# Kernel optimization log

Hardware: AMD Instinct MI355X
Metric: run time of the kernel (lower is better)

## Reference

```python
import jax, jax.numpy as jnp
import numpy as np
from jax import lax

DIST_THRESH = 180.0
ATT_THRESH = 0.05


def setup_inputs() -> dict:
    key = jax.random.key(0)
    ks = jax.random.split(key, 6)
    B, N, H, W = 16, 512, 25, 25
    F, Fh = H * W, int(H * W * 1.5)  # 625, 937
    x4 = jax.random.normal(ks[0], (B, N, H, W), dtype=jnp.float32) * 0.25
    attention = jax.random.uniform(ks[1], (B, N, 1, 1), dtype=jnp.float32)
    W1 = jax.random.normal(ks[2], (2, F, Fh), dtype=jnp.float32) * (1.0 / np.sqrt(F))
    b1 = jnp.zeros((Fh,), dtype=jnp.float32)
    W2 = jax.random.normal(ks[3], (2, Fh, F), dtype=jnp.float32) * (1.0 / np.sqrt(Fh))
    b2 = jnp.zeros((F,), dtype=jnp.float32)
    return {"x4": x4, "attention": attention, "W1": W1, "b1": b1, "W2": W2, "b2": b2}


def _build_adjacency(X, att):
    """X: [B,N,F] node features, att: [B,N]. Returns thresholded adjacency [B,N,N]."""
    B, N, F = X.shape
    # pairwise L1 distances, row-by-row scan to avoid materializing [B,N,N,F]
    Xs = jnp.swapaxes(X, 0, 1)  # [N,B,F]

    def row(_, xi):  # xi: [B,F]
        d = jnp.sum(jnp.abs(xi[:, None, :] - X), axis=-1)  # [B,N]
        return None, d

    _, D = lax.scan(row, None, Xs)          # [N,B,N]
    D = jnp.swapaxes(D, 0, 1)               # [B,N,N]
    att_d = jnp.abs(att[:, :, None] - att[:, None, :])  # [B,N,N]
    A = ((D <= DIST_THRESH) & (att_d <= ATT_THRESH)).astype(jnp.float32)
    # original only fills i<j and j<i, diagonal stays 0
    A = A * (1.0 - jnp.eye(N, dtype=jnp.float32))
    return A


def _process_graph(A):
    """A + I, then row-normalize by inverse degree (D^-1 (A+I))."""
    N = A.shape[1]
    A = A + jnp.eye(N, dtype=A.dtype)
    deg = jnp.sum(A, axis=-1)               # [B,N]
    dinv = jnp.where(deg > 0, 1.0 / deg, 0.0)
    return dinv[:, :, None] * A


def _cheb_conv(x, L, Wk, b):
    """ChebConv with K=2 over dense normalized graph L: T0=x, T1=Lx."""
    t1 = jnp.einsum('bij,bjf->bif', L, x)
    return jnp.einsum('bnf,fo->bno', x, Wk[0]) + jnp.einsum('bnf,fo->bno', t1, Wk[1]) + b


def reference(x4, attention, W1, b1, W2, b2):
    B, N, H, W = x4.shape
    X = x4.reshape(B, N, H * W)             # [B,N,625] flow_x
    att = attention[:, :, 0, 0]             # [B,N]
    A = _build_adjacency(X, att)
    L = _process_graph(A)
    h = jax.nn.relu(_cheb_conv(X, L, W1, b1))   # [B,N,937]
    out = jax.nn.relu(_cheb_conv(h, L, W2, b2))  # [B,N,625]
    return out
```

## Files before the change

### kernel.cpp

```cpp
#include <hip/hip_runtime.h>
#include <stdint.h>

typedef uint16_t u16;
typedef uint32_t u32;
typedef __attribute__((ext_vector_type(4))) float f32x4;
typedef __attribute__((ext_vector_type(4))) unsigned short us4;
typedef __attribute__((ext_vector_type(8))) unsigned short us8;

#define NB   16
#define NN   512
#define FF   625
#define FH   937
#define ROWS 8192
#define KS1  1280
#define KS2  1920
#define NPX  640
#define NPH  960
#define F4   160
#define ITILE 8

using frag_ab = __attribute__((ext_vector_type(8))) short;
using frag_cd = __attribute__((ext_vector_type(4))) float;

__device__ __forceinline__ u16 f32_bf16(float f) {
  union { float f; uint32_t u; } x; x.f = f;
  uint32_t r = x.u + 0x7fffu + ((x.u >> 16) & 1u);
  return (u16)(r >> 16);
}
__device__ __forceinline__ void gload_lds16(const void* g, void* l) {
  __builtin_amdgcn_global_load_lds((__attribute__((address_space(1))) void*)g,
                                   (__attribute__((address_space(3))) void*)l,
                                   16, 0, 0);
}

__global__ __launch_bounds__(256) void prep(
    const float* __restrict__ x4, const float* __restrict__ att,
    const float* __restrict__ W1, const float* __restrict__ W2,
    f32x4* __restrict__ Xpad, u16* __restrict__ Xcat, u16* __restrict__ Xt,
    u16* __restrict__ W1t, u16* __restrict__ W2t,
    float* __restrict__ att_s, u16* __restrict__ ord_g)
{
  const int blk = blockIdx.x;
  const int tid = threadIdx.x;
  if (blk < 4096) {
    const int xcd = blk & 7, loc = blk >> 3;
    const int row0 = xcd * 1024 + loc * 2;
    for (int s = tid; s < 320; s += 256) {
      const int row = row0 + (s >= 160);
      const int k4 = (s >= 160) ? s - 160 : s;
      f32x4 v; us4 o;
      #pragma unroll
      for (int t = 0; t < 4; ++t) {
        const int f = k4 * 4 + t;
        float x = (f < FF) ? x4[(size_t)row * FF + f] : 0.f;
        v[t] = x; o[t] = f32_bf16(x);
      }
      Xpad[(size_t)row * F4 + k4] = v;
      *(us4*)(Xcat + (size_t)row * KS1 + k4 * 4) = o;
    }
  } else if (blk < 9216) {
    __shared__ float tile[32][33];
    const int bb = blk - 4096;
    const int xcd = bb & 7, sub = bb >> 3;
    const int b = xcd * 2 + sub / 320;
    const int t = sub % 320;
    const int ft = t % 20, kt = t / 20;
    const int tx = tid & 31, ty = tid >> 5;
    #pragma unroll
    for (int r = 0; r < 4; ++r) {
      const int node = kt * 32 + ty + r * 8;
      const int f = ft * 32 + tx;
      tile[ty + r * 8][tx] = (f < FF) ? x4[((size_t)b * NN + node) * FF + f] : 0.f;
    }
    __syncthreads();
    #pragma unroll
    for (int r = 0; r < 4; ++r) {
      const int f = ft * 32 + ty + r * 8;
      const int node = kt * 32 + tx;
      Xt[((size_t)b * NPX + f) * 512 + node] = f32_bf16(tile[tx][ty + r * 8]);
    }
  } else if (blk < 10496) {
    __shared__ float tile[32][33];
    const int bb = blk - 9216;
    const int kt = bb % 40, nt = bb / 40;
    const int tx = tid & 31, ty = tid >> 5;
    #pragma unroll
    for (int r = 0; r < 4; ++r) {
      int k = kt * 32 + ty + r * 8;
      int n = nt * 32 + tx;
      float v = 0.f;
      int c = -1, kk = 0;
      if (k < 625) { c = 0; kk = k; }
      else if (k >= 640 && k < 1265) { c = 1; kk = k - 640; }
      if (c >= 0 && n < FH) v = W1[((size_t)c * 625 + kk) * FH + n];
      tile[ty + r * 8][tx] = v;
    }
    __syncthreads();
    #pragma unroll
    for (int r = 0; r < 4; ++r) {
      int n = nt * 32 + ty + r * 8;
      int k = kt * 32 + tx;
      W1t[(size_t)n * KS1 + k] = f32_bf16(tile[tx][ty + r * 8]);
    }
  } else if (blk < 11696) {
    __shared__ float tile[32][33];
    const int bb = blk - 10496;
    const int kt = bb % 60, nt = bb / 60;
    const int tx = tid & 31, ty = tid >> 5;
    #pragma unroll
    for (int r = 0; r < 4; ++r) {
      int k = kt * 32 + ty + r * 8;
      int n = nt * 32 + tx;
      float v = 0.f;
      int c = -1, kk = 0;
      if (k < 937) { c = 0; kk = k; }
      else if (k >= 960 && k < 1897) { c = 1; kk = k - 960; }
      if (c >= 0 && n < FF) v = W2[((size_t)c * 937 + kk) * FF + n];
      tile[ty + r * 8][tx] = v;
    }
    __syncthreads();
    #pragma unroll
    for (int r = 0; r < 4; ++r) {
      int n = nt * 32 + ty + r * 8;
      int k = kt * 32 + tx;
      W2t[(size_t)n * KS2 + k] = f32_bf16(tile[tx][ty + r * 8]);
    }
  } else {
    __shared__ float sa[512];
    __shared__ u16 so[512];
    const int b = blk - 11696;
    sa[tid] = att[b * NN + tid]; sa[tid + 256] = att[b * NN + tid + 256];
    so[tid] = (u16)tid; so[tid + 256] = (u16)(tid + 256);
    for (int k = 2; k <= 512; k <<= 1) {
      for (int j = k >> 1; j > 0; j >>= 1) {
        __syncthreads();
        const int i = ((tid & ~(j - 1)) << 1) | (tid & (j - 1));
        const int p = i | j;
        const bool up = ((i & k) == 0);
        const float va = sa[i], vp = sa[p];
        if ((va > vp) == up) {
          sa[i] = vp; sa[p] = va;
          const u16 t = so[i]; so[i] = so[p]; so[p] = t;
        }
      }
    }
    __syncthreads();
    att_s[b * NN + tid] = sa[tid]; att_s[b * NN + tid + 256] = sa[tid + 256];
    ord_g[b * NN + tid] = so[tid]; ord_g[b * NN + tid + 256] = so[tid + 256];
  }
}

__global__ __launch_bounds__(256) void build_L_tiled(
    const f32x4* __restrict__ Xpad,
    const float* __restrict__ att_s, const u16* __restrict__ ord_g,
    u16* __restrict__ L)
{
  __shared__ f32x4 Xi[ITILE][F4];
  __shared__ float as_[512];
  __shared__ u16 ord[512];
  __shared__ u32 mask[ITILE][16];
  __shared__ int deg[ITILE];
  __shared__ int jlo_s, jhi_s;
  __shared__ u16 dvs[ITILE];

  const int tid = threadIdx.x;
  const int blk = blockIdx.x;
  const int xcd = blk & 7, sub = blk >> 3;
  const int b = xcd * 2 + (sub >> 6);
  const int it = sub & 63;
  const int s0 = it * ITILE;
  const f32x4* Xb4 = Xpad + (size_t)b * NN * F4;

  as_[tid] = att_s[b * NN + tid]; as_[tid + 256] = att_s[b * NN + tid + 256];
  ord[tid] = ord_g[b * NN + tid]; ord[tid + 256] = ord_g[b * NN + tid + 256];
  if (tid < ITILE * 16) ((u32*)mask)[tid] = 0;
  if (tid < ITILE) deg[tid] = 0;
  __syncthreads();

  for (int s = tid; s < ITILE * F4; s += 256) {
    const int ii = s / F4, k4 = s - ii * F4;
    Xi[ii][k4] = Xb4[(size_t)ord[s0 + ii] * F4 + k4];
  }
  if (tid == 0) {
    const float lot = as_[s0] - 0.05f;
    int lo = 0, hi = 512;
    while (lo < hi) { int m = (lo + hi) >> 1; if (as_[m] < lot) lo = m + 1; else hi = m; }
    jlo_s = lo;
  } else if (tid == 1) {
    const float hit = as_[s0 + ITILE - 1] + 0.05f;
    int lo = 0, hi = 512;
    while (lo < hi) { int m = (lo + hi) >> 1; if (as_[m] <= hit) lo = m + 1; else hi = m; }
    jhi_s = lo;
  }
  __syncthreads();

  const int hl = tid & 31;
  const int hw = tid >> 5;
  const int jlo = jlo_s, jhi = jhi_s;

  for (int sj = jlo + hw; sj < jhi; sj += 8) {
    const int oj = ord[sj];
    const f32x4* Xj = Xb4 + (size_t)oj * F4;
    const f32x4 xj0 = Xj[hl];
    const f32x4 xj1 = Xj[32 + hl];
    const f32x4 xj2 = Xj[64 + hl];
    const f32x4 xj3 = Xj[96 + hl];
    const f32x4 xj4 = Xj[128 + hl];
    const float aj = as_[sj];
    #pragma unroll 2
    for (int ii = 0; ii < ITILE; ++ii) {
      const int si = s0 + ii;
      if (si == sj || fabsf(aj - as_[si]) > 0.05f) continue;
      const f32x4 d0 = Xi[ii][hl] - xj0;
      const f32x4 d1 = Xi[ii][32 + hl] - xj1;
      const f32x4 d2 = Xi[ii][64 + hl] - xj2;
      const f32x4 d3 = Xi[ii][96 + hl] - xj3;
      const f32x4 d4 = Xi[ii][128 + hl] - xj4;
      float p = 0.f;
      #pragma unroll
      for (int t = 0; t < 4; ++t)
        p += fabsf(d0[t]) + fabsf(d1[t]) + fabsf(d2[t]) + fabsf(d3[t]) + fabsf(d4[t]);
      #pragma unroll
      for (int off = 16; off; off >>= 1) p += __shfl_xor(p, off, 64);
      if (hl == 0 && p <= 180.0f) {
        atomicOr(&mask[ii][sj >> 5], 1u << (sj & 31));
        atomicAdd(&deg[ii], 1);
      }
    }
  }
  __syncthreads();

  if (tid < ITILE) dvs[tid] = f32_bf16(1.0f / (float)(deg[tid] + 1));
  __syncthreads();

  if (tid < ITILE * 16) {
    const int ii = tid >> 4, w = tid & 15;
    const int oi = ord[s0 + ii];
    u16* Lrow = L + ((size_t)b * 512 + oi) * 512;
    const u16 dv = dvs[ii];
    u32 m = mask[ii][w];
    while (m) {
      const int bit = __ffs(m) - 1;
      m &= m - 1;
      Lrow[ord[w * 32 + bit]] = dv;
    }
    if (w == 0) Lrow[oi] = dv;
  }
}

template <int KS, int NTILE, int NREAL, int NSTORE, bool RELU, bool BIAS,
          bool OUT_BF16, bool TSTORE>
__device__ __forceinline__ void gemm_core(
    const u16* __restrict__ At, const u16* __restrict__ Btt,
    const float* __restrict__ bias, void* __restrict__ C,
    u16* __restrict__ tbuf, long crow0, int col0, int ldc)
{
  constexpr int NI = NTILE / 32;
  constexpr int BR = NTILE / 32;
  __shared__ __align__(16) u16 Ash[128 * 64];
  __shared__ __align__(16) u16 Bsh[NTILE * 64];

  const int tid  = threadIdx.x;
  const int lane = tid & 63;
  const int wave = tid >> 6;
  const int wm = wave & 1, wn = wave >> 1;
  const int q = lane >> 4, l16 = lane & 15;

  const u16* pa[4]; const u16* pb[BR];
  #pragma unroll
  for (int r = 0; r < 4; ++r) {
    const int ci = r * 256 + tid;
    const int row = ci >> 3, cpos = ci & 7;
    pa[r] = At + (size_t)row * KS + (cpos ^ (row & 7)) * 8;
  }
  #pragma unroll
  for (int r = 0; r < BR; ++r) {
    const int ci = r * 256 + tid;
    const int row = ci >> 3, cpos = ci & 7;
    pb[r] = Btt + (size_t)row * KS + (cpos ^ (row & 7)) * 8;
  }
  const int wbase = (tid & 192) * 8;

  const frag_ab* fA[4][2]; const frag_ab* fB[NI][2];
  #pragma unroll
  for (int mi = 0; mi < 4; ++mi) {
    const int row = wm * 64 + mi * 16 + l16;
    fA[mi][0] = (const frag_ab*)&Ash[row * 64 + ((q    ) ^ (l16 & 7)) * 8];
    fA[mi][1] = (const frag_ab*)&Ash[row * 64 + ((q + 4) ^ (l16 & 7)) * 8];
  }
  #pragma unroll
  for (int ni = 0; ni < NI; ++ni) {
    const int row = wn * (NTILE / 2) + ni * 16 + l16;
    fB[ni][0] = (const frag_ab*)&Bsh[row * 64 + ((q    ) ^ (l16 & 7)) * 8];
    fB[ni][1] = (const frag_ab*)&Bsh[row * 64 + ((q + 4) ^ (l16 & 7)) * 8];
  }

  frag_cd acc[4][NI] = {};

  constexpr int KT = KS / 64;
  for (int kt = 0; kt < KT; ++kt) {
    __syncthreads();
    #pragma unroll
    for (int r = 0; r < 4; ++r) { gload_lds16(pa[r], &Ash[r * 2048 + wbase]); pa[r] += 64; }
    #pragma unroll
    for (int r = 0; r < BR; ++r) { gload_lds16(pb[r], &Bsh[r * 2048 + wbase]); pb[r] += 64; }
    __syncthreads();

    #pragma unroll
    for (int kk = 0; kk < 2; ++kk) {
      frag_ab av[4], bv[NI];
      #pragma unroll
      for (int mi = 0; mi < 4; ++mi) av[mi] = *fA[mi][kk];
      #pragma unroll
      for (int ni = 0; ni < NI; ++ni) bv[ni] = *fB[ni][kk];
      #pragma unroll
      for (int mi = 0; mi < 4; ++mi)
        #pragma unroll
        for (int ni = 0; ni < NI; ++ni)
          acc[mi][ni] = __builtin_amdgcn_mfma_f32_16x16x32_bf16(
              av[mi], bv[ni], acc[mi][ni], 0, 0, 0);
    }
  }

  #pragma unroll
  for (int ni = 0; ni < NI; ++ni) {
    const int col = col0 + wn * (NTILE / 2) + ni * 16 + l16;
    if (col >= NSTORE) continue;
    const bool ok = (col < NREAL);
    float bvv = 0.f;
    if (BIAS) bvv = ok ? bias[col] : 0.f;
    #pragma unroll
    for (int mi = 0; mi < 4; ++mi) {
      #pragma unroll
      for (int r = 0; r < 4; ++r) {
        const long rowg = crow0 + wm * 64 + mi * 16 + q * 4 + r;
        float v = acc[mi][ni][r];
        if (BIAS) v += bvv;
        if (RELU) v = fmaxf(v, 0.f);
        if (!ok) v = 0.f;
        if (OUT_BF16) ((u16*)C)[rowg * (size_t)ldc + col] = f32_bf16(v);
        else          ((float*)C)[rowg * (size_t)ldc + col] = v;
        if (TSTORE) {
          tbuf[((size_t)(rowg >> 9) * NPH + col) * 512 + (rowg & 511)] = f32_bf16(v);
        }
      }
    }
  }
}

template <int KS, int NTILE, int NREAL, int NSTORE, bool RELU, bool BIAS,
          bool OUT_BF16, bool TSTORE>
__global__ __launch_bounds__(256) void gemm_dense(
    const u16* __restrict__ A, const u16* __restrict__ Bt,
    const float* __restrict__ bias, void* __restrict__ C,
    u16* __restrict__ tbuf, int ldc)
{
  const int x = blockIdx.x;
  const int mt = ((x & 7) << 3) | (x >> 3);
  gemm_core<KS, NTILE, NREAL, NSTORE, RELU, BIAS, OUT_BF16, TSTORE>(
      A + (size_t)mt * 128 * KS, Bt + (size_t)blockIdx.y * NTILE * KS,
      bias, C, tbuf, (long)mt * 128, blockIdx.y * NTILE, ldc);
}

template <int NP>
__global__ __launch_bounds__(256) void spmm(
    const u16* __restrict__ L, const u16* __restrict__ Bt,
    u16* __restrict__ C, int ldc)
{
  constexpr int TPB = 4 * (NP / 64);
  const int blk = blockIdx.x;
  const int xcd = blk & 7, sub = blk >> 3;
  const int b = xcd * 2 + sub / TPB;
  const int t = sub % TPB;
  const int mt = t & 3, nt = t >> 2;
  gemm_core<512, 64, NP, NP, false, false, true, false>(
      L + ((size_t)b * 512 + mt * 128) * 512,
      Bt + ((size_t)b * NP + nt * 64) * 512,
      nullptr, C, nullptr, (long)b * 512 + mt * 128, nt * 64, ldc);
}

extern "C" void kernel_launch(void* const* d_in, const int* in_sizes, int n_in,
                              void* d_out, int out_size, void* d_ws, size_t ws_size,
                              hipStream_t stream) {
  const float* x4  = (const float*)d_in[0];
  const float* att = (const float*)d_in[1];
  const float* W1  = (const float*)d_in[2];
  const float* b1  = (const float*)d_in[3];
  const float* W2  = (const float*)d_in[4];
  const float* b2  = (const float*)d_in[5];
  float* out = (float*)d_out;

  char* ws = (char*)d_ws;
  f32x4* Xpad = (f32x4*)ws;
  u16* ht = (u16*)ws;       ws += (size_t)ROWS * F4 * 16;
  u16* Xcat = (u16*)ws;  ws += (size_t)ROWS * KS1 * 2;
  u16* hcat = (u16*)ws;  ws += (size_t)ROWS * KS2 * 2;
  u16* W1t  = (u16*)ws;  ws += (size_t)1024 * KS1 * 2;
  u16* W2t  = (u16*)ws;  ws += (size_t)640 * KS2 * 2;
  u16* Lm   = (u16*)ws;  ws += (size_t)NB * 512 * 512 * 2;
  u16* Xt   = (u16*)ws;  ws += (size_t)NB * NPX * 512 * 2;
  float* att_s = (float*)ws; ws += (size_t)NB * NN * 4;
  u16* ord_g   = (u16*)ws;   ws += (size_t)NB * NN * 2;

  prep<<<dim3(11712), 256, 0, stream>>>(x4, att, W1, W2, Xpad, Xcat, Xt,
                                        W1t, W2t, att_s, ord_g);
  hipMemsetAsync(Lm, 0, (size_t)NB * 512 * 512 * 2, stream);
  build_L_tiled<<<dim3(1024), 256, 0, stream>>>(Xpad, att_s, ord_g, Lm);
  spmm<NPX><<<dim3(640), 256, 0, stream>>>(Lm, Xt, Xcat + NPX, KS1);
  gemm_dense<KS1, 128, FH, NPH, true, true, true, true>
      <<<dim3(64, 8), 256, 0, stream>>>(Xcat, W1t, b1, (void*)hcat, ht, KS2);
  spmm<NPH><<<dim3(960), 256, 0, stream>>>(Lm, ht, hcat + NPH, KS2);
  gemm_dense<KS2, 64, FF, FF, true, true, false, false>
      <<<dim3(64, 10), 256, 0, stream>>>(hcat, W2t, b2, (void*)out, nullptr, FF);
}
```

Measured before the change: 238.0 us.

## Restructure prep, L construction and h transpose to cut memory traffic

Folds the Xpad/Xcat conversion into the x4 transpose tiles so x4 is read once. The adjacency builder now uses 4-row tiles across twice as many blocks and batches the warp reductions across rows. Each block writes its full L rows densely through an inverse permutation, which removes the separate memset. The strided transposed store of h is moved out of the first dense GEMM epilogue into a dedicated LDS-tiled transpose kernel. This trades an extra launch and an extra pass over h for coalesced writes and less redundant work.

```diff
diff --git a/kernel.cpp b/kernel.cpp
--- a/kernel.cpp
+++ b/kernel.cpp
@@ -5,7 +5,6 @@
 typedef uint32_t u32;
 typedef __attribute__((ext_vector_type(4))) float f32x4;
 typedef __attribute__((ext_vector_type(4))) unsigned short us4;
-typedef __attribute__((ext_vector_type(8))) unsigned short us8;
 
 #define NB   16
 #define NN   512
@@ -17,7 +16,7 @@
 #define NPX  640
 #define NPH  960
 #define F4   160
-#define ITILE 8
+#define ITILE 4
 
 using frag_ab = __attribute__((ext_vector_type(8))) short;
 using frag_cd = __attribute__((ext_vector_type(4))) float;
@@ -42,26 +41,9 @@
 {
   const int blk = blockIdx.x;
   const int tid = threadIdx.x;
-  if (blk < 4096) {
-    const int xcd = blk & 7, loc = blk >> 3;
-    const int row0 = xcd * 1024 + loc * 2;
-    for (int s = tid; s < 320; s += 256) {
-      const int row = row0 + (s >= 160);
-      const int k4 = (s >= 160) ? s - 160 : s;
-      f32x4 v; us4 o;
-      #pragma unroll
-      for (int t = 0; t < 4; ++t) {
-        const int f = k4 * 4 + t;
-        float x = (f < FF) ? x4[(size_t)row * FF + f] : 0.f;
-        v[t] = x; o[t] = f32_bf16(x);
-      }
-      Xpad[(size_t)row * F4 + k4] = v;
-      *(us4*)(Xcat + (size_t)row * KS1 + k4 * 4) = o;
-    }
-  } else if (blk < 9216) {
+  if (blk < 5120) {
     __shared__ float tile[32][33];
-    const int bb = blk - 4096;
-    const int xcd = bb & 7, sub = bb >> 3;
+    const int xcd = blk & 7, sub = blk >> 3;
     const int b = xcd * 2 + sub / 320;
     const int t = sub % 320;
     const int ft = t % 20, kt = t / 20;
@@ -79,9 +61,19 @@
       const int node = kt * 32 + tx;
       Xt[((size_t)b * NPX + f) * 512 + node] = f32_bf16(tile[tx][ty + r * 8]);
     }
-  } else if (blk < 10496) {
+    const int nd = tid >> 3, sl = tid & 7;
+    const int row = b * NN + kt * 32 + nd;
+    f32x4 v; us4 o;
+    #pragma unroll
+    for (int t2 = 0; t2 < 4; ++t2) {
+      const float x = tile[nd][sl * 4 + t2];
+      v[t2] = x; o[t2] = f32_bf16(x);
+    }
+    Xpad[(size_t)row * F4 + ft * 8 + sl] = v;
+    *(us4*)(Xcat + (size_t)row * KS1 + ft * 32 + sl * 4) = o;
+  } else if (blk < 6400) {
     __shared__ float tile[32][33];
-    const int bb = blk - 9216;
+    const int bb = blk - 5120;
     const int kt = bb % 40, nt = bb / 40;
     const int tx = tid & 31, ty = tid >> 5;
     #pragma unroll
@@ -102,9 +94,9 @@
       int k = kt * 32 + tx;
       W1t[(size_t)n * KS1 + k] = f32_bf16(tile[tx][ty + r * 8]);
     }
-  } else if (blk < 11696) {
+  } else if (blk < 7600) {
     __shared__ float tile[32][33];
-    const int bb = blk - 10496;
+    const int bb = blk - 6400;
     const int kt = bb % 60, nt = bb / 60;
     const int tx = tid & 31, ty = tid >> 5;
     #pragma unroll
@@ -128,7 +120,7 @@
   } else {
     __shared__ float sa[512];
     __shared__ u16 so[512];
-    const int b = blk - 11696;
+    const int b = blk - 7600;
     sa[tid] = att[b * NN + tid]; sa[tid + 256] = att[b * NN + tid + 256];
     so[tid] = (u16)tid; so[tid + 256] = (u16)(tid + 256);
     for (int k = 2; k <= 512; k <<= 1) {
@@ -158,21 +150,23 @@
   __shared__ f32x4 Xi[ITILE][F4];
   __shared__ float as_[512];
   __shared__ u16 ord[512];
+  __shared__ u16 inv[512];
   __shared__ u32 mask[ITILE][16];
   __shared__ int deg[ITILE];
   __shared__ int jlo_s, jhi_s;
-  __shared__ u16 dvs[ITILE];
 
   const int tid = threadIdx.x;
   const int blk = blockIdx.x;
   const int xcd = blk & 7, sub = blk >> 3;
-  const int b = xcd * 2 + (sub >> 6);
-  const int it = sub & 63;
+  const int b = xcd * 2 + (sub >> 7);
+  const int it = sub & 127;
   const int s0 = it * ITILE;
   const f32x4* Xb4 = Xpad + (size_t)b * NN * F4;
 
   as_[tid] = att_s[b * NN + tid]; as_[tid + 256] = att_s[b * NN + tid + 256];
-  ord[tid] = ord_g[b * NN + tid]; ord[tid + 256] = ord_g[b * NN + tid + 256];
+  const u16 o0 = ord_g[b * NN + tid], o1 = ord_g[b * NN + tid + 256];
+  ord[tid] = o0; ord[tid + 256] = o1;
+  inv[o0] = (u16)tid; inv[o1] = (u16)(tid + 256);
   if (tid < ITILE * 16) ((u32*)mask)[tid] = 0;
   if (tid < ITILE) deg[tid] = 0;
   __syncthreads();
@@ -199,18 +193,16 @@
   const int jlo = jlo_s, jhi = jhi_s;
 
   for (int sj = jlo + hw; sj < jhi; sj += 8) {
-    const int oj = ord[sj];
-    const f32x4* Xj = Xb4 + (size_t)oj * F4;
+    const f32x4* Xj = Xb4 + (size_t)ord[sj] * F4;
     const f32x4 xj0 = Xj[hl];
     const f32x4 xj1 = Xj[32 + hl];
     const f32x4 xj2 = Xj[64 + hl];
     const f32x4 xj3 = Xj[96 + hl];
     const f32x4 xj4 = Xj[128 + hl];
     const float aj = as_[sj];
-    #pragma unroll 2
+    f32x4 pv;
+    #pragma unroll
     for (int ii = 0; ii < ITILE; ++ii) {
-      const int si = s0 + ii;
-      if (si == sj || fabsf(aj - as_[si]) > 0.05f) continue;
       const f32x4 d0 = Xi[ii][hl] - xj0;
       const f32x4 d1 = Xi[ii][32 + hl] - xj1;
       const f32x4 d2 = Xi[ii][64 + hl] - xj2;
@@ -220,40 +212,48 @@
       #pragma unroll
       for (int t = 0; t < 4; ++t)
         p += fabsf(d0[t]) + fabsf(d1[t]) + fabsf(d2[t]) + fabsf(d3[t]) + fabsf(d4[t]);
-      #pragma unroll
-      for (int off = 16; off; off >>= 1) p += __shfl_xor(p, off, 64);
-      if (hl == 0 && p <= 180.0f) {
-        atomicOr(&mask[ii][sj >> 5], 1u << (sj & 31));
-        atomicAdd(&deg[ii], 1);
+      pv[ii] = p;
+    }
+    #pragma unroll
+    for (int off = 16; off; off >>= 1) {
+      f32x4 o;
+      o[0] = __shfl_xor(pv[0], off, 64);
+      o[1] = __shfl_xor(pv[1], off, 64);
+      o[2] = __shfl_xor(pv[2], off, 64);
+      o[3] = __shfl_xor(pv[3], off, 64);
+      pv += o;
+    }
+    if (hl == 0) {
+      #pragma unroll
+      for (int ii = 0; ii < ITILE; ++ii) {
+        const int si = s0 + ii;
+        if (si != sj && fabsf(aj - as_[si]) <= 0.05f && pv[ii] <= 180.0f) {
+          atomicOr(&mask[ii][sj >> 5], 1u << (sj & 31));
+          atomicAdd(&deg[ii], 1);
+        }
       }
     }
   }
   __syncthreads();
 
-  if (tid < ITILE) dvs[tid] = f32_bf16(1.0f / (float)(deg[tid] + 1));
-  __syncthreads();
-
-  if (tid < ITILE * 16) {
-    const int ii = tid >> 4, w = tid & 15;
+  #pragma unroll
+  for (int ii = 0; ii < ITILE; ++ii) {
     const int oi = ord[s0 + ii];
+    const u16 dv = f32_bf16(1.0f / (float)(deg[ii] + 1));
     u16* Lrow = L + ((size_t)b * 512 + oi) * 512;
-    const u16 dv = dvs[ii];
-    u32 m = mask[ii][w];
-    while (m) {
-      const int bit = __ffs(m) - 1;
-      m &= m - 1;
-      Lrow[ord[w * 32 + bit]] = dv;
-    }
-    if (w == 0) Lrow[oi] = dv;
-  }
-}
-
-template <int KS, int NTILE, int NREAL, int NSTORE, bool RELU, bool BIAS,
-          bool OUT_BF16, bool TSTORE>
+    const int j0 = 2 * tid;
+    const int sA = inv[j0], sB = inv[j0 + 1];
+    const u32 fA = (j0 == oi)     | ((mask[ii][sA >> 5] >> (sA & 31)) & 1u);
+    const u32 fB = (j0 + 1 == oi) | ((mask[ii][sB >> 5] >> (sB & 31)) & 1u);
+    *(u32*)(Lrow + j0) = (fA ? (u32)dv : 0u) | ((fB ? (u32)dv : 0u) << 16);
+  }
+}
+
+template <int KS, int NTILE, int NREAL, int NSTORE, bool RELU, bool BIAS, bool OUT_BF16>
 __device__ __forceinline__ void gemm_core(
     const u16* __restrict__ At, const u16* __restrict__ Btt,
     const float* __restrict__ bias, void* __restrict__ C,
-    u16* __restrict__ tbuf, long crow0, int col0, int ldc)
+    long crow0, int col0, int ldc)
 {
   constexpr int NI = NTILE / 32;
   constexpr int BR = NTILE / 32;
@@ -340,26 +340,21 @@
         if (!ok) v = 0.f;
         if (OUT_BF16) ((u16*)C)[rowg * (size_t)ldc + col] = f32_bf16(v);
         else          ((float*)C)[rowg * (size_t)ldc + col] = v;
-        if (TSTORE) {
-          tbuf[((size_t)(rowg >> 9) * NPH + col) * 512 + (rowg & 511)] = f32_bf16(v);
-        }
       }
     }
   }
 }
 
-template <int KS, int NTILE, int NREAL, int NSTORE, bool RELU, bool BIAS,
-          bool OUT_BF16, bool TSTORE>
+template <int KS, int NTILE, int NREAL, int NSTORE, bool RELU, bool BIAS, bool OUT_BF16>
 __global__ __launch_bounds__(256) void gemm_dense(
     const u16* __restrict__ A, const u16* __restrict__ Bt,
-    const float* __restrict__ bias, void* __restrict__ C,
-    u16* __restrict__ tbuf, int ldc)
+    const float* __restrict__ bias, void* __restrict__ C, int ldc)
 {
   const int x = blockIdx.x;
   const int mt = ((x & 7) << 3) | (x >> 3);
-  gemm_core<KS, NTILE, NREAL, NSTORE, RELU, BIAS, OUT_BF16, TSTORE>(
+  gemm_core<KS, NTILE, NREAL, NSTORE, RELU, BIAS, OUT_BF16>(
       A + (size_t)mt * 128 * KS, Bt + (size_t)blockIdx.y * NTILE * KS,
-      bias, C, tbuf, (long)mt * 128, blockIdx.y * NTILE, ldc);
+      bias, C, (long)mt * 128, blockIdx.y * NTILE, ldc);
 }
 
 template <int NP>
@@ -373,10 +368,36 @@
   const int b = xcd * 2 + sub / TPB;
   const int t = sub % TPB;
   const int mt = t & 3, nt = t >> 2;
-  gemm_core<512, 64, NP, NP, false, false, true, false>(
+  gemm_core<512, 64, NP, NP, false, false, true>(
       L + ((size_t)b * 512 + mt * 128) * 512,
       Bt + ((size_t)b * NP + nt * 64) * 512,
-      nullptr, C, nullptr, (long)b * 512 + mt * 128, nt * 64, ldc);
+      nullptr, C, (long)b * 512 + mt * 128, nt * 64, ldc);
+}
+
+__global__ __launch_bounds__(256) void transpose_h(
+    const u16* __restrict__ hcat, u16* __restrict__ ht)
+{
+  __shared__ u16 tile[32][34];
+  const int blk = blockIdx.x;
+  const int xcd = blk & 7, sub = blk >> 3;
+  const int b = xcd * 2 + sub / 480;
+  const int t = sub % 480;
+  const int kt = t % 16, nt = t / 16;
+  const int tid = threadIdx.x;
+  const int tx = tid & 31, ty = tid >> 5;
+  #pragma unroll
+  for (int r = 0; r < 4; ++r) {
+    const int node = kt * 32 + ty + r * 8;
+    const int n = nt * 32 + tx;
+    tile[ty + r * 8][tx] = hcat[((size_t)b * NN + node) * KS2 + n];
+  }
+  __syncthreads();
+  #pragma unroll
+  for (int r = 0; r < 4; ++r) {
+    const int n = nt * 32 + ty + r * 8;
+    const int node = kt * 32 + tx;
+    ht[((size_t)b * NPH + n) * 512 + node] = tile[tx][ty + r * 8];
+  }
 }
 
 extern "C" void kernel_launch(void* const* d_in, const int* in_sizes, int n_in,
@@ -402,14 +423,14 @@
   float* att_s = (float*)ws; ws += (size_t)NB * NN * 4;
   u16* ord_g   = (u16*)ws;   ws += (size_t)NB * NN * 2;
 
-  prep<<<dim3(11712), 256, 0, stream>>>(x4, att, W1, W2, Xpad, Xcat, Xt,
-                                        W1t, W2t, att_s, ord_g);
-  hipMemsetAsync(Lm, 0, (size_t)NB * 512 * 512 * 2, stream);
-  build_L_tiled<<<dim3(1024), 256, 0, stream>>>(Xpad, att_s, ord_g, Lm);
+  prep<<<dim3(7616), 256, 0, stream>>>(x4, att, W1, W2, Xpad, Xcat, Xt,
+                                       W1t, W2t, att_s, ord_g);
+  build_L_tiled<<<dim3(2048), 256, 0, stream>>>(Xpad, att_s, ord_g, Lm);
   spmm<NPX><<<dim3(640), 256, 0, stream>>>(Lm, Xt, Xcat + NPX, KS1);
-  gemm_dense<KS1, 128, FH, NPH, true, true, true, true>
-      <<<dim3(64, 8), 256, 0, stream>>>(Xcat, W1t, b1, (void*)hcat, ht, KS2);
+  gemm_dense<KS1, 128, FH, NPH, true, true, true>
+      <<<dim3(64, 8), 256, 0, stream>>>(Xcat, W1t, b1, (void*)hcat, KS2);
+  transpose_h<<<dim3(7680), 256, 0, stream>>>(hcat, ht);
   spmm<NPH><<<dim3(960), 256, 0, stream>>>(Lm, ht, hcat + NPH, KS2);
-  gemm_dense<KS2, 64, FF, FF, true, true, false, false>
-      <<<dim3(64, 10), 256, 0, stream>>>(hcat, W2t, b2, (void*)out, nullptr, FF);
-}
+  gemm_dense<KS2, 64, FF, FF, true, true, false>
+      <<<dim3(64, 10), 256, 0, stream>>>(hcat, W2t, b2, (void*)out, FF);
+}
```

New measurement: 229.8 us. 1.04x faster.
